# Kernel tuning notes

Hardware: AMD Instinct MI355X
Metric: run time of the kernel (lower is better)

The kernel has to match this reference:

```python
import jax, jax.numpy as jnp
import numpy as np

B, S, WL = 128, 128, 16
V, C, T = 50000, 100, 17
WE, CE, CF, K, H = 300, 50, 50, 3, 256
D = WE + CF  # LSTM input dim


def setup_inputs() -> dict:
    key = jax.random.key(0)
    ks = jax.random.split(key, 16)
    def n(k, shape, scale=0.05):
        return jax.random.normal(k, shape, jnp.float32) * scale
    words = jax.random.randint(ks[0], (B, S), 0, V)
    chars = jax.random.randint(ks[1], (B, S, WL), 0, C)
    tags = jax.random.randint(ks[2], (B, S), 0, T)
    lengths = jax.random.randint(ks[3], (B,), 1, S + 1)  # at least 1 valid token
    return dict(
        words=words, chars=chars, tags=tags, lengths=lengths,
        word_emb=n(ks[4], (V, WE)).at[0].set(0.0),  # padding_idx=0
        char_emb=n(ks[5], (C, CE)),
        conv_w=n(ks[6], (CF, CE, K)), conv_b=jnp.zeros((CF,), jnp.float32),
        w_ih_f=n(ks[7], (4 * H, D)), w_hh_f=n(ks[8], (4 * H, H)), b_f=jnp.zeros((4 * H,), jnp.float32),
        w_ih_b=n(ks[9], (4 * H, D)), w_hh_b=n(ks[10], (4 * H, H)), b_b=jnp.zeros((4 * H,), jnp.float32),
        proj_w=n(ks[11], (T, 2 * H)), proj_b=jnp.zeros((T,), jnp.float32),
        trans=n(ks[12], (T, T), 0.1), start_trans=n(ks[13], (T,), 0.1), end_trans=n(ks[14], (T,), 0.1),
    )


def _lstm(x, mask, w_ih, w_hh, b):
    # x: [B,S,D], mask: [B,S] bool. PyTorch gate order: i, f, g, o.
    Bh = w_hh.shape[1]
    xg = jnp.einsum('bsd,gd->bsg', x, w_ih) + b  # [B,S,4H]
    def step(carry, inp):
        h, c = carry
        gx, m = inp  # [B,4H], [B]
        g = gx + h @ w_hh.T
        i, f, gg, o = jnp.split(g, 4, axis=-1)
        i = jax.nn.sigmoid(i); f = jax.nn.sigmoid(f)
        gg = jnp.tanh(gg); o = jax.nn.sigmoid(o)
        cn = f * c + i * gg
        hn = o * jnp.tanh(cn)
        m_ = m[:, None]
        return (jnp.where(m_, hn, h), jnp.where(m_, cn, c)), hn * m_
    b_ = x.shape[0]
    init = (jnp.zeros((b_, Bh), x.dtype), jnp.zeros((b_, Bh), x.dtype))
    _, hs = jax.lax.scan(step, init, (jnp.swapaxes(xg, 0, 1), jnp.swapaxes(mask, 0, 1)))
    return jnp.swapaxes(hs, 0, 1)  # [B,S,H]


def _reverse_valid(x, lengths):
    # reverse only the first `length` entries of each row (pack_padded semantics)
    s = x.shape[1]
    t = jnp.arange(s)[None, :]
    idx = jnp.where(t < lengths[:, None], lengths[:, None] - 1 - t, t)
    return jnp.take_along_axis(x, idx[:, :, None], axis=1)


def _crf_nll(emissions, tags, lengths, trans, start_trans, end_trans):
    b, s, t_ = emissions.shape
    mask = jnp.arange(s)[None, :] < lengths[:, None]  # [B,S]
    maskf = mask.astype(emissions.dtype)
    # gold path score
    emit_sc = jnp.take_along_axis(emissions, tags[:, :, None], axis=2)[:, :, 0]  # [B,S]
    score = start_trans[tags[:, 0]] + (emit_sc * maskf).sum(1)
    tr = trans[tags[:, :-1], tags[:, 1:]]  # [B,S-1]
    score = score + (tr * maskf[:, 1:]).sum(1)
    last = jnp.take_along_axis(tags, (lengths - 1)[:, None], axis=1)[:, 0]
    score = score + end_trans[last]
    # partition function (forward algorithm)
    alpha0 = start_trans[None, :] + emissions[:, 0]  # [B,T]
    def step(alpha, inp):
        emit, m = inp  # [B,T], [B]
        nxt = jax.scipy.special.logsumexp(alpha[:, :, None] + trans[None] + emit[:, None, :], axis=1)
        return jnp.where(m[:, None], nxt, alpha), None
    alpha, _ = jax.lax.scan(step, alpha0,
                            (jnp.swapaxes(emissions[:, 1:], 0, 1), jnp.swapaxes(mask[:, 1:], 0, 1)))
    logZ = jax.scipy.special.logsumexp(alpha + end_trans[None, :], axis=-1)
    return jnp.sum(logZ - score)


def reference(words, chars, tags, lengths, word_emb, char_emb, conv_w, conv_b,
              w_ih_f, w_hh_f, b_f, w_ih_b, w_hh_b, b_b, proj_w, proj_b,
              trans, start_trans, end_trans):
    b, s = words.shape
    wl = chars.shape[2]
    we = word_emb[words]  # [B,S,WE]
    ce = char_emb[chars]  # [B,S,WL,CE]
    # CharCNN: conv over word-length, relu, max-pool
    x = ce.reshape(b * s, wl, -1).transpose(0, 2, 1)  # [B*S, CE, WL]
    conv = jax.lax.conv_general_dilated(x, conv_w, (1,), 'SAME',
                                        dimension_numbers=('NCH', 'OIH', 'NCH'))
    conv = conv + conv_b[None, :, None]
    cf = jnp.max(jax.nn.relu(conv), axis=-1).reshape(b, s, -1)  # [B,S,CF]
    inp = jnp.concatenate([we, cf], axis=2)  # [B,S,WE+CF]
    mask = jnp.arange(s)[None, :] < lengths[:, None]
    fwd = _lstm(inp, mask, w_ih_f, w_hh_f, b_f)
    bwd = _reverse_valid(_lstm(_reverse_valid(inp, lengths), mask, w_ih_b, w_hh_b, b_b), lengths)
    h = jnp.concatenate([fwd, bwd], axis=2)  # [B,S,2H]
    emissions = jnp.einsum('bsh,th->bst', h, proj_w) + proj_b
    return _crf_nll(emissions, tags, lengths, trans, start_trans, end_trans)
```

## Files before the change

### kernel.cpp

```cpp
#include <hip/hip_runtime.h>
#include <stdint.h>

typedef unsigned char u8;
typedef unsigned short u16;
typedef unsigned int u32;
typedef unsigned long long u64;

#define NPOS 16384
#define KPAD 384

typedef __attribute__((ext_vector_type(8))) short bf16x8;
typedef __attribute__((ext_vector_type(4))) float f32x4;
typedef __attribute__((ext_vector_type(8))) int i32x8;

__device__ __forceinline__ float bf2f(u16 u) { return __uint_as_float(((u32)u) << 16); }
__device__ __forceinline__ u16 f2bf(float f) {
    u32 u = __float_as_uint(f);
    u += 0x7fffu + ((u >> 16) & 1u);
    return (u16)(u >> 16);
}
__device__ __forceinline__ float frcp(float x) {
#if __has_builtin(__builtin_amdgcn_rcpf)
    return __builtin_amdgcn_rcpf(x);
#else
    return 1.0f / x;
#endif
}
__device__ __forceinline__ float sigm(float x) { return frcp(1.0f + __expf(-x)); }
__device__ __forceinline__ float tanh_(float x) { return fmaf(2.0f, frcp(1.0f + __expf(-2.0f * x)), -1.0f); }

__device__ u8 f2fp8_manual(float f) {
    u32 u = __float_as_uint(f);
    u32 s = (u >> 31) << 7;
    u32 ae = (u >> 23) & 255u;
    u32 m = u & 0x7fffffu;
    int e = (int)ae - 127;
    if (ae == 0) return (u8)s;
    if (e >= 9) return (u8)(s | 0x7e);
    if (e >= -6) {
        u32 mant = m >> 20;
        u32 rem = m & 0xfffffu;
        if (rem > 0x80000u || (rem == 0x80000u && (mant & 1u))) mant++;
        u32 ef = (u32)(e + 7);
        if (mant == 8u) { mant = 0u; ef++; }
        if (ef >= 16u || (ef == 15u && mant == 7u)) return (u8)(s | 0x7e);
        return (u8)(s | (ef << 3) | mant);
    }
    if (e < -10) return (u8)s;
    int sb = 14 - e;
    u32 X = 0x800000u | m;
    u32 mant = X >> sb;
    u32 rem = X & ((1u << sb) - 1u);
    u32 half = 1u << (sb - 1);
    if (rem > half || (rem == half && (mant & 1u))) mant++;
    if (mant >= 8u) return (u8)(s | (1u << 3));
    return (u8)(s | mant);
}

__device__ __forceinline__ u32 f2fp8(float f) {
#if __has_builtin(__builtin_amdgcn_cvt_pk_fp8_f32)
    return (u32)(__builtin_amdgcn_cvt_pk_fp8_f32(f, f, 0, false) & 0xff);
#else
    return (u32)f2fp8_manual(f);
#endif
}

static constexpr size_t OFF_INP  = 0;
static constexpr size_t OFF_WIH  = 12582912;
static constexpr size_t OFF_WHH  = 14155776;
static constexpr size_t OFF_XG   = 15204352;
static constexpr size_t OFF_HS   = 82313216;
static constexpr size_t OFF_EMIS = 99090432;
static constexpr size_t OFF_NLL  = 100204544;

__global__ __launch_bounds__(128) void k_prep_wih(const float* __restrict__ wf,
                                                  const float* __restrict__ wb,
                                                  u16* __restrict__ wih) {
    int n = blockIdx.x, tid = threadIdx.x;
    const float* src = (n < 1024) ? (wf + (size_t)n * 350) : (wb + (size_t)(n - 1024) * 350);
    u16* dst = wih + (size_t)n * KPAD;
    for (int k = tid; k < KPAD; k += 128) dst[k] = (k < 350) ? f2bf(src[k]) : (u16)0;
}

__global__ __launch_bounds__(128) void k_prep_whh8(const float* __restrict__ wf,
                                                   const float* __restrict__ wb,
                                                   u8* __restrict__ whh8) {
    int bx = blockIdx.x, tid = threadIdx.x;
    int d = bx >> 10, row = bx & 1023;
    const float* src = (d ? wb : wf) + (size_t)row * 256;
    int g = row >> 8, hid = row & 255;
    int w = hid >> 5, nb = (hid >> 4) & 1, c16 = hid & 15;
    u8* base = whh8 + ((size_t)((d * 8 + w) * 4 + g)) * 8192;
    for (int k = tid; k < 256; k += 128) {
        int kk = k >> 7, q = (k >> 5) & 3, j = k & 31;
        base[((nb * 2 + kk) * 64 + (q * 16 + c16)) * 32 + j] = f2fp8_manual(src[k]);
    }
}

__global__ __launch_bounds__(128) void k_embed_conv(const int* __restrict__ words,
                                                    const int* __restrict__ chars,
                                                    const float* __restrict__ word_emb,
                                                    const float* __restrict__ char_emb,
                                                    const float* __restrict__ conv_w,
                                                    const float* __restrict__ conv_b,
                                                    u16* __restrict__ inp) {
    int pos = blockIdx.x, tid = threadIdx.x;
    __shared__ float ce[18 * 50];
    const int* ch = chars + (size_t)pos * 16;
    for (int i = tid; i < 18 * 50; i += 128) {
        int row = i / 50, c = i - row * 50;
        float v = 0.f;
        if (row >= 1 && row <= 16) v = char_emb[(size_t)ch[row - 1] * 50 + c];
        ce[i] = v;
    }
    __syncthreads();
    {
        const float4* we4 = (const float4*)(word_emb + (size_t)words[pos] * 300);
        u16* op = inp + (size_t)pos * KPAD;
        if (tid < 75) {
            float4 v = we4[tid];
            u64 pk = (u64)f2bf(v.x) | ((u64)f2bf(v.y) << 16) |
                     ((u64)f2bf(v.z) << 32) | ((u64)f2bf(v.w) << 48);
            *(u64*)(op + tid * 4) = pk;
        }
        for (int c = 350 + tid; c < KPAD; c += 128) op[c] = 0;
    }
    if (tid < 100) {
        int oc = tid >> 1, half = tid & 1, t0 = half * 8;
        float acc[8];
#pragma unroll
        for (int tt = 0; tt < 8; ++tt) acc[tt] = 0.f;
        const float* wrow = conv_w + (size_t)oc * 150;
        for (int ic = 0; ic < 50; ++ic) {
#pragma unroll
            for (int k = 0; k < 3; ++k) {
                float wv = wrow[ic * 3 + k];
#pragma unroll
                for (int tt = 0; tt < 8; ++tt)
                    acc[tt] = fmaf(ce[(t0 + tt + k) * 50 + ic], wv, acc[tt]);
            }
        }
        float cb = conv_b[oc];
        float m = 0.f;
#pragma unroll
        for (int tt = 0; tt < 8; ++tt) m = fmaxf(m, acc[tt] + cb);
        m = fmaxf(m, __shfl_xor(m, 1));
        if (half == 0) inp[(size_t)pos * KPAD + 300 + oc] = f2bf(m);
    }
}

__global__ __launch_bounds__(256, 2) void k_gemm(const u16* __restrict__ A,
                                                 const u16* __restrict__ Bm,
                                                 u16* __restrict__ C,
                                                 const int* __restrict__ lengths,
                                                 const float* __restrict__ bias_f,
                                                 const float* __restrict__ bias_b) {
    __shared__ u16 sa[128 * 64];
    __shared__ u16 sb[128 * 64];
    int tid = threadIdx.x;
    int dd = blockIdx.x >> 3, hblk = blockIdx.x & 7;
    int m0 = blockIdx.y * 128;
    int lane = tid & 63, wid = tid >> 6;
    int wr = wid >> 1, wc = wid & 1;
    f32x4 acc[4][4];
#pragma unroll
    for (int mt = 0; mt < 4; ++mt)
#pragma unroll
        for (int g = 0; g < 4; ++g) acc[mt][g] = (f32x4){0.f, 0.f, 0.f, 0.f};

    for (int kt = 0; kt < 6; ++kt) {
#pragma unroll
        for (int c = 0; c < 4; ++c) {
            int idx = (c * 256 + tid) * 16;
            int row = idx >> 7, colb = idx & 127;
            int dst = idx ^ ((row & 7) << 4);
            uint4 va = *(const uint4*)((const char*)A + (size_t)(m0 + row) * 768 + kt * 128 + colb);
            *(uint4*)((char*)sa + dst) = va;
            int bmrow = dd * 1024 + (row >> 5) * 256 + hblk * 32 + (row & 31);
            uint4 vb = *(const uint4*)((const char*)Bm + (size_t)bmrow * 768 + kt * 128 + colb);
            *(uint4*)((char*)sb + dst) = vb;
        }
        __syncthreads();
#pragma unroll
        for (int kc = 0; kc < 2; ++kc) {
            bf16x8 af[4], bf[4];
#pragma unroll
            for (int mt = 0; mt < 4; ++mt) {
                int row = wr * 64 + mt * 16 + (lane & 15);
                int off = (row * 128 + kc * 64 + (lane >> 4) * 16) ^ ((row & 7) << 4);
                af[mt] = *(const bf16x8*)((const char*)sa + off);
            }
#pragma unroll
            for (int g = 0; g < 4; ++g) {
                int row = g * 32 + wc * 16 + (lane & 15);
                int off = (row * 128 + kc * 64 + (lane >> 4) * 16) ^ ((row & 7) << 4);
                bf[g] = *(const bf16x8*)((const char*)sb + off);
            }
#pragma unroll
            for (int mt = 0; mt < 4; ++mt)
#pragma unroll
                for (int g = 0; g < 4; ++g)
                    acc[mt][g] = __builtin_amdgcn_mfma_f32_16x16x32_bf16(af[mt], bf[g], acc[mt][g], 0, 0, 0);
        }
        __syncthreads();
    }
    int b = blockIdx.y;
    int len = lengths[b];
    int grp = b >> 4, row16 = b & 15;
    int qq = row16 >> 2, rg = row16 & 3;
    int c16 = lane & 15;
    int hid = hblk * 32 + wc * 16 + c16;
    const float* bias = dd ? bias_b : bias_f;
    float bv[4];
#pragma unroll
    for (int g = 0; g < 4; ++g) bv[g] = bias[g * 256 + hid];
    u32 base16 = (u32)((hblk * 64 + qq * 16 + c16) * 32 + (wc * 4 + rg) * 4);
    size_t slab0 = ((size_t)(dd * 8 + grp) * 128) * 16384;
#pragma unroll
    for (int mt = 0; mt < 4; ++mt)
#pragma unroll
        for (int r = 0; r < 4; ++r) {
            int t = wr * 64 + mt * 16 + (lane >> 4) * 4 + r;
            int tt = dd ? ((t < len) ? (len - 1 - t) : t) : t;
            u64 pk = (u64)f2bf(acc[mt][0][r] + bv[0]) |
                     ((u64)f2bf(acc[mt][1][r] + bv[1]) << 16) |
                     ((u64)f2bf(acc[mt][2][r] + bv[2]) << 32) |
                     ((u64)f2bf(acc[mt][3][r] + bv[3]) << 48);
            *(u64*)(C + slab0 + (size_t)tt * 16384 + base16) = pk;
        }
}

#define LSTM_STEP(T, XC, XN, HA, HW)                                              \
    {                                                                             \
        *(uint4*)(&XN[0])  = *(const uint4*)(xp);                                 \
        *(uint4*)(&XN[4])  = *(const uint4*)(xp + 8);                             \
        *(uint4*)(&XN[8])  = *(const uint4*)(xp + 16);                            \
        *(uint4*)(&XN[12]) = *(const uint4*)(xp + 24);                            \
        xp += 16384;                                                              \
        f32x4 acc[8];                                                             \
        _Pragma("unroll") for (int nb = 0; nb < 2; ++nb)                          \
            _Pragma("unroll") for (int rg = 0; rg < 4; ++rg) {                    \
                int u = nb * 4 + rg;                                              \
                u32 w0 = XC[u * 2], w1 = XC[u * 2 + 1];                           \
                acc[nb * 4 + 0][rg] = __uint_as_float(w0 << 16);                  \
                acc[nb * 4 + 1][rg] = __uint_as_float(w0 & 0xffff0000u);          \
                acc[nb * 4 + 2][rg] = __uint_as_float(w1 << 16);                  \
                acc[nb * 4 + 3][rg] = __uint_as_float(w1 & 0xffff0000u);          \
            }                                                                     \
        i32x8 a0, a1;                                                             \
        *(uint4*)&a0       = *(const uint4*)(HA);                                 \
        *((uint4*)&a0 + 1) = *(const uint4*)(HA + 16);                            \
        *(uint4*)&a1       = *(const uint4*)(HA + 128);                           \
        *((uint4*)&a1 + 1) = *(const uint4*)(HA + 144);                           \
        __builtin_amdgcn_s_setprio(1);                                            \
        _Pragma("unroll") for (int g = 0; g < 4; ++g)                             \
            acc[g] = __builtin_amdgcn_mfma_scale_f32_16x16x128_f8f6f4(            \
                a0, br[g * 4 + 0], acc[g], 0, 0, 0, 127, 0, 127);                 \
        _Pragma("unroll") for (int g = 0; g < 4; ++g)                             \
            acc[g] = __builtin_amdgcn_mfma_scale_f32_16x16x128_f8f6f4(            \
                a1, br[g * 4 + 1], acc[g], 0, 0, 0, 127, 0, 127);                 \
        _Pragma("unroll") for (int g = 0; g < 4; ++g)                             \
            acc[4 + g] = __builtin_amdgcn_mfma_scale_f32_16x16x128_f8f6f4(        \
                a0, br[g * 4 + 2], acc[4 + g], 0, 0, 0, 127, 0, 127);             \
        _Pragma("unroll") for (int g = 0; g < 4; ++g)                             \
            acc[4 + g] = __builtin_amdgcn_mfma_scale_f32_16x16x128_f8f6f4(        \
                a1, br[g * 4 + 3], acc[4 + g], 0, 0, 0, 127, 0, 127);             \
        __builtin_amdgcn_s_setprio(0);                                            \
        _Pragma("unroll") for (int rg = 0; rg < 4; ++rg) {                        \
            bool mv = (T) < lenr[rg];                                             \
            _Pragma("unroll") for (int nb = 0; nb < 2; ++nb) {                    \
                int u = nb * 4 + rg;                                              \
                float gi = sigm(acc[nb * 4 + 0][rg]);                             \
                float gf = sigm(acc[nb * 4 + 1][rg]);                             \
                float gg = tanh_(acc[nb * 4 + 2][rg]);                            \
                float go = sigm(acc[nb * 4 + 3][rg]);                             \
                float cn = gf * cst[u] + gi * gg;                                 \
                float hn = go * tanh_(cn);                                        \
                cst[u] = mv ? cn : cst[u];                                        \
                hbf[u] = mv ? (__float_as_uint(hn) >> 16) : hbf[u];               \
                hq[u]  = mv ? f2fp8(hn) : hq[u];                                  \
                voff[u] += mv ? dstepB : 0;                                       \
                *(u16*)(hsp + voff[u]) = (u16)hbf[u];                             \
                (HW)[rg * 272 + nb * 16] = (u8)hq[u];                             \
            }                                                                     \
        }                                                                         \
        asm volatile("s_waitcnt lgkmcnt(0)\n\ts_barrier" ::: "memory");           \
    }

__global__ __launch_bounds__(512, 2) void k_lstm(const u16* __restrict__ xg2,
                                                 const u8* __restrict__ whh8,
                                                 const int* __restrict__ lengths,
                                                 u16* __restrict__ hs) {
    __shared__ u8 h8[2][4352];
    int tid = threadIdx.x, lane = tid & 63, w = tid >> 6;
    int bx = blockIdx.x;
    int d = bx >> 3, grp = bx & 7;
    int c16 = lane & 15, q = lane >> 4;

    u8* hflat = &h8[0][0];
    for (int i = tid * 8; i < 8704; i += 4096) *(u64*)(hflat + i) = 0;

    int lenr[4];
#pragma unroll
    for (int rg = 0; rg < 4; ++rg) lenr[rg] = lengths[grp * 16 + q * 4 + rg];

    const u8* wbse = whh8 + ((size_t)((d * 8 + w) * 4)) * 8192;
    i32x8 br[16];
#pragma unroll
    for (int g = 0; g < 4; ++g)
#pragma unroll
        for (int nb = 0; nb < 2; ++nb)
#pragma unroll
            for (int kk = 0; kk < 2; ++kk) {
                const u8* p = wbse + (size_t)g * 8192 + ((nb * 2 + kk) * 64 + lane) * 32;
                i32x8 v;
                *(uint4*)&v       = *(const uint4*)p;
                *((uint4*)&v + 1) = *(const uint4*)(p + 16);
                br[g * 4 + nb * 2 + kk] = v;
            }

    float cst[8];
    u32 hq[8], hbf[8];
#pragma unroll
    for (int u = 0; u < 8; ++u) { cst[u] = 0.f; hq[u] = 0; hbf[u] = 0; }

    u32 voff[8];
    int dstepB = d ? -1024 : 1024;
    u8* hsp = (u8*)hs;
#pragma unroll
    for (int nb = 0; nb < 2; ++nb)
#pragma unroll
        for (int rg = 0; rg < 4; ++rg) {
            int u = nb * 4 + rg;
            int row = q * 4 + rg;
            int hid = w * 32 + nb * 16 + c16;
            int p0 = d ? (lenr[rg] - 1) : 0;
            voff[u] = (u32)((((grp * 16 + row) * 128 + p0) * 512 + d * 256 + hid) * 2 - dstepB);
        }

    const u16* xslab = xg2 + ((size_t)(d * 8 + grp) * 128) * 16384 + (w * 64 + lane) * 32;
    u32 xqa[16], xqb[16];
    *(uint4*)(&xqa[0])  = *(const uint4*)(xslab);
    *(uint4*)(&xqa[4])  = *(const uint4*)(xslab + 8);
    *(uint4*)(&xqa[8])  = *(const uint4*)(xslab + 16);
    *(uint4*)(&xqa[12]) = *(const uint4*)(xslab + 24);
    const u16* xp = xslab + 16384;

    const u8* ha0 = hflat + (c16 * 272 + q * 32);
    const u8* ha1 = ha0 + 4352;
    u8* hw1 = hflat + (q * 1088 + w * 32 + c16);
    u8* hw0 = hw1 + 4352;

    __syncthreads();

    for (int t2 = 0; t2 < 128; t2 += 2) {
        LSTM_STEP(t2,     xqa, xqb, ha0, hw0)
        LSTM_STEP(t2 + 1, xqb, xqa, ha1, hw1)
    }
}

__global__ __launch_bounds__(256) void k_emis(const u16* __restrict__ hs,
                                              const float* __restrict__ proj_w,
                                              const float* __restrict__ proj_b,
                                              float* __restrict__ emis) {
    __shared__ float pw[17 * 512];
    int tid = threadIdx.x;
    for (int i = tid; i < 17 * 512; i += 256) pw[i] = proj_w[i];
    __syncthreads();
    int lane = tid & 63, wv = tid >> 6;
    int pos = blockIdx.x * 4 + wv;
    float hv[8];
    const u16* hp = hs + (size_t)pos * 512 + lane * 8;
#pragma unroll
    for (int j = 0; j < 8; ++j) hv[j] = bf2f(hp[j]);
    for (int tg = 0; tg < 17; ++tg) {
        const float* wp = pw + tg * 512 + lane * 8;
        float s = 0.f;
#pragma unroll
        for (int j = 0; j < 8; ++j) s = fmaf(hv[j], wp[j], s);
#pragma unroll
        for (int off = 32; off; off >>= 1) s += __shfl_down(s, off);
        if (lane == 0) emis[(size_t)pos * 17 + tg] = s + proj_b[tg];
    }
}

__global__ __launch_bounds__(64) void k_crf(const float* __restrict__ emis,
                                            const int* __restrict__ tags,
                                            const int* __restrict__ lengths,
                                            const float* __restrict__ trans,
                                            const float* __restrict__ start_trans,
                                            const float* __restrict__ end_trans,
                                            float* __restrict__ nll) {
    int b = blockIdx.x, lane = threadIdx.x;
    __shared__ float tr[289];
    __shared__ float al[17];
    __shared__ float scs;
    for (int i = lane; i < 289; i += 64) tr[i] = trans[i];
    int len = lengths[b];
    const int* tg = tags + (size_t)b * 128;
    const float* em = emis + (size_t)b * 128 * 17;
    __syncthreads();

    float sc = 0.f;
    for (int t = lane; t < len; t += 64) {
        sc += em[t * 17 + tg[t]];
        if (t >= 1) sc += tr[tg[t - 1] * 17 + tg[t]];
    }
#pragma unroll
    for (int off = 32; off; off >>= 1) sc += __shfl_down(sc, off);
    if (lane == 0) scs = sc + start_trans[tg[0]] + end_trans[tg[len - 1]];

    if (lane < 17) al[lane] = start_trans[lane] + em[lane];
    __syncthreads();
    for (int t = 1; t < len; ++t) {
        float anew = 0.f;
        if (lane < 17) {
            float m = -1e30f;
            for (int i = 0; i < 17; ++i) m = fmaxf(m, al[i] + tr[i * 17 + lane]);
            float s = 0.f;
            for (int i = 0; i < 17; ++i) s += __expf(al[i] + tr[i * 17 + lane] - m);
            anew = m + __logf(s) + em[t * 17 + lane];
        }
        __syncthreads();
        if (lane < 17) al[lane] = anew;
        __syncthreads();
    }
    float v = (lane < 17) ? al[lane] + end_trans[lane] : -1e30f;
    float m = v;
#pragma unroll
    for (int off = 32; off; off >>= 1) m = fmaxf(m, __shfl_xor(m, off));
    float s = (lane < 17) ? __expf(v - m) : 0.f;
#pragma unroll
    for (int off = 32; off; off >>= 1) s += __shfl_xor(s, off);
    if (lane == 0) nll[b] = (m + __logf(s)) - scs;
}

__global__ __launch_bounds__(128) void k_reduce(const float* __restrict__ nll, float* __restrict__ out) {
    int tid = threadIdx.x;
    float v = nll[tid];
#pragma unroll
    for (int off = 32; off; off >>= 1) v += __shfl_down(v, off);
    __shared__ float partial[2];
    if ((tid & 63) == 0) partial[tid >> 6] = v;
    __syncthreads();
    if (tid == 0) out[0] = partial[0] + partial[1];
}

extern "C" void kernel_launch(void* const* d_in, const int* in_sizes, int n_in,
                              void* d_out, int out_size, void* d_ws, size_t ws_size,
                              hipStream_t stream) {
    (void)in_sizes; (void)n_in; (void)out_size; (void)ws_size;
    const int*   words       = (const int*)d_in[0];
    const int*   chars       = (const int*)d_in[1];
    const int*   tags        = (const int*)d_in[2];
    const int*   lengths     = (const int*)d_in[3];
    const float* word_emb    = (const float*)d_in[4];
    const float* char_emb    = (const float*)d_in[5];
    const float* conv_w      = (const float*)d_in[6];
    const float* conv_b      = (const float*)d_in[7];
    const float* w_ih_f      = (const float*)d_in[8];
    const float* w_hh_f      = (const float*)d_in[9];
    const float* b_f         = (const float*)d_in[10];
    const float* w_ih_b      = (const float*)d_in[11];
    const float* w_hh_b      = (const float*)d_in[12];
    const float* b_b         = (const float*)d_in[13];
    const float* proj_w      = (const float*)d_in[14];
    const float* proj_b      = (const float*)d_in[15];
    const float* trans       = (const float*)d_in[16];
    const float* start_trans = (const float*)d_in[17];
    const float* end_trans   = (const float*)d_in[18];

    char* ws = (char*)d_ws;
    u16* inp   = (u16*)(ws + OFF_INP);
    u16* wih   = (u16*)(ws + OFF_WIH);
    u8*  whh8  = (u8*)(ws + OFF_WHH);
    u16* xgb   = (u16*)(ws + OFF_XG);
    u16* hsb   = (u16*)(ws + OFF_HS);
    float* em  = (float*)(ws + OFF_EMIS);
    float* nll = (float*)(ws + OFF_NLL);

    k_prep_wih<<<2048, 128, 0, stream>>>(w_ih_f, w_ih_b, wih);
    k_prep_whh8<<<2048, 128, 0, stream>>>(w_hh_f, w_hh_b, whh8);
    k_embed_conv<<<NPOS, 128, 0, stream>>>(words, chars, word_emb, char_emb, conv_w, conv_b, inp);
    k_gemm<<<dim3(16, 128), 256, 0, stream>>>(inp, wih, xgb, lengths, b_f, b_b);
    k_lstm<<<16, 512, 0, stream>>>(xgb, whh8, lengths, hsb);
    k_emis<<<4096, 256, 0, stream>>>(hsb, proj_w, proj_b, em);
    k_crf<<<128, 64, 0, stream>>>(em, tags, lengths, trans, start_trans, end_trans, nll);
    k_reduce<<<1, 128, 0, stream>>>(nll, (float*)d_out);
}
```

Baseline: 479.8 us.

## Fuse weight prep with embedding/conv front kernel and batch emission positions

Merges the two weight-preparation kernels and the embedding/char-CNN kernel into one launch. Each block now handles 8 positions, using a transposed conv weight table and a transposed char-embedding tile in shared memory, so each thread computes two output channels over all 16 time steps. The emission kernel processes 4 positions per wave with vectorised loads, which amortises the shuffle reductions and the loads of projection weights. This cuts launch count and per-block setup in exchange for more register pressure in the conv loop. It also adds a small transpose kernel that reuses the XG workspace region before the GEMM writes into it.

```diff
diff --git a/kernel.cpp b/kernel.cpp
--- a/kernel.cpp
+++ b/kernel.cpp
@@ -72,80 +72,129 @@
 static constexpr size_t OFF_HS   = 82313216;
 static constexpr size_t OFF_EMIS = 99090432;
 static constexpr size_t OFF_NLL  = 100204544;
-
-__global__ __launch_bounds__(128) void k_prep_wih(const float* __restrict__ wf,
-                                                  const float* __restrict__ wb,
-                                                  u16* __restrict__ wih) {
-    int n = blockIdx.x, tid = threadIdx.x;
-    const float* src = (n < 1024) ? (wf + (size_t)n * 350) : (wb + (size_t)(n - 1024) * 350);
-    u16* dst = wih + (size_t)n * KPAD;
-    for (int k = tid; k < KPAD; k += 128) dst[k] = (k < 350) ? f2bf(src[k]) : (u16)0;
-}
-
-__global__ __launch_bounds__(128) void k_prep_whh8(const float* __restrict__ wf,
-                                                   const float* __restrict__ wb,
-                                                   u8* __restrict__ whh8) {
-    int bx = blockIdx.x, tid = threadIdx.x;
-    int d = bx >> 10, row = bx & 1023;
-    const float* src = (d ? wb : wf) + (size_t)row * 256;
-    int g = row >> 8, hid = row & 255;
-    int w = hid >> 5, nb = (hid >> 4) & 1, c16 = hid & 15;
-    u8* base = whh8 + ((size_t)((d * 8 + w) * 4 + g)) * 8192;
-    for (int k = tid; k < 256; k += 128) {
-        int kk = k >> 7, q = (k >> 5) & 3, j = k & 31;
-        base[((nb * 2 + kk) * 64 + (q * 16 + c16)) * 32 + j] = f2fp8_manual(src[k]);
-    }
-}
-
-__global__ __launch_bounds__(128) void k_embed_conv(const int* __restrict__ words,
-                                                    const int* __restrict__ chars,
-                                                    const float* __restrict__ word_emb,
-                                                    const float* __restrict__ char_emb,
-                                                    const float* __restrict__ conv_w,
-                                                    const float* __restrict__ conv_b,
-                                                    u16* __restrict__ inp) {
-    int pos = blockIdx.x, tid = threadIdx.x;
-    __shared__ float ce[18 * 50];
-    const int* ch = chars + (size_t)pos * 16;
-    for (int i = tid; i < 18 * 50; i += 128) {
-        int row = i / 50, c = i - row * 50;
-        float v = 0.f;
-        if (row >= 1 && row <= 16) v = char_emb[(size_t)ch[row - 1] * 50 + c];
-        ce[i] = v;
+static constexpr size_t OFF_WT   = OFF_XG;
+
+__global__ __launch_bounds__(256) void k_prep0(const float* __restrict__ conv_w,
+                                               float* __restrict__ wt) {
+    int idx = blockIdx.x * 256 + threadIdx.x;
+    if (idx < 7500) {
+        int oc = idx / 150, r = idx - oc * 150;
+        wt[r * 52 + oc] = conv_w[oc * 150 + r];
+    }
+}
+
+__global__ __launch_bounds__(256) void k_front(const int* __restrict__ words,
+                                               const int* __restrict__ chars,
+                                               const float* __restrict__ word_emb,
+                                               const float* __restrict__ char_emb,
+                                               const float* __restrict__ wt,
+                                               const float* __restrict__ conv_b,
+                                               u16* __restrict__ inp,
+                                               const float* __restrict__ wihf,
+                                               const float* __restrict__ wihb,
+                                               u16* __restrict__ wih,
+                                               const float* __restrict__ whf,
+                                               const float* __restrict__ whb,
+                                               u8* __restrict__ whh8) {
+    __shared__ float ce_t[8][50][20];
+    int b = blockIdx.x, tid = threadIdx.x;
+
+    if (b >= 2048) {
+        if (b < 3072) {
+            int n = (b - 2048) * 2 + (tid >> 7);
+            int t128 = tid & 127;
+            const float* src = (n < 1024) ? (wihf + (size_t)n * 350) : (wihb + (size_t)(n - 1024) * 350);
+            u16* dst = wih + (size_t)n * KPAD;
+            for (int k = t128; k < KPAD; k += 128) dst[k] = (k < 350) ? f2bf(src[k]) : (u16)0;
+        } else {
+            int gr = (b - 3072) * 2 + (tid >> 7);
+            int t128 = tid & 127;
+            int d = gr >> 10, row = gr & 1023;
+            const float* src = (d ? whb : whf) + (size_t)row * 256;
+            int g = row >> 8, hid = row & 255;
+            int w = hid >> 5, nb = (hid >> 4) & 1, c16 = hid & 15;
+            u8* base = whh8 + ((size_t)((d * 8 + w) * 4 + g)) * 8192;
+            for (int k = t128; k < 256; k += 128) {
+                int kk = k >> 7, q = (k >> 5) & 3, j = k & 31;
+                base[((nb * 2 + kk) * 64 + (q * 16 + c16)) * 32 + j] = f2fp8_manual(src[k]);
+            }
+        }
+        return;
+    }
+
+    int pos0 = b * 8;
+
+    if (tid < 128) {
+        int p = tid >> 4, c = tid & 15;
+        int ch = chars[(size_t)(pos0 + p) * 16 + c];
+        const float* src = char_emb + (size_t)ch * 50;
+#pragma unroll
+        for (int i = 0; i < 25; ++i) {
+            float2 v = *(const float2*)(src + i * 2);
+            ce_t[p][i * 2][c + 1] = v.x;
+            ce_t[p][i * 2 + 1][c + 1] = v.y;
+        }
+    } else {
+        int base = tid - 128;
+        for (int i = base; i < 1600; i += 128) {
+            int p = i / 200, rem = i - p * 200;
+            int ic = rem >> 2, cid = rem & 3;
+            ce_t[p][ic][cid == 0 ? 0 : 16 + cid] = 0.f;
+        }
+    }
+
+    for (int r = 0; r < 3; ++r) {
+        int idx = r * 256 + tid;
+        if (idx < 600) {
+            int p = idx / 75, v = idx - p * 75;
+            const float4* we4 = (const float4*)(word_emb + (size_t)words[pos0 + p] * 300);
+            float4 val = we4[v];
+            u64 pk = (u64)f2bf(val.x) | ((u64)f2bf(val.y) << 16) |
+                     ((u64)f2bf(val.z) << 32) | ((u64)f2bf(val.w) << 48);
+            *(u64*)(inp + (size_t)(pos0 + p) * KPAD + v * 4) = pk;
+        }
+    }
+    {
+        int idx = tid;
+        if (idx < 136) {
+            int p = idx / 17, j = idx - p * 17;
+            *(u32*)(inp + (size_t)(pos0 + p) * KPAD + 350 + 2 * j) = 0;
+        }
     }
     __syncthreads();
-    {
-        const float4* we4 = (const float4*)(word_emb + (size_t)words[pos] * 300);
-        u16* op = inp + (size_t)pos * KPAD;
-        if (tid < 75) {
-            float4 v = we4[tid];
-            u64 pk = (u64)f2bf(v.x) | ((u64)f2bf(v.y) << 16) |
-                     ((u64)f2bf(v.z) << 32) | ((u64)f2bf(v.w) << 48);
-            *(u64*)(op + tid * 4) = pk;
-        }
-        for (int c = 350 + tid; c < KPAD; c += 128) op[c] = 0;
-    }
-    if (tid < 100) {
-        int oc = tid >> 1, half = tid & 1, t0 = half * 8;
-        float acc[8];
-#pragma unroll
-        for (int tt = 0; tt < 8; ++tt) acc[tt] = 0.f;
-        const float* wrow = conv_w + (size_t)oc * 150;
+
+    if (tid < 200) {
+        int p = tid / 25, ocp = tid - p * 25;
+        int oc = ocp * 2;
+        float acc0[16], acc1[16];
+#pragma unroll
+        for (int t = 0; t < 16; ++t) { acc0[t] = 0.f; acc1[t] = 0.f; }
+        const float* cebase = &ce_t[p][0][0];
         for (int ic = 0; ic < 50; ++ic) {
+            float c[20];
+            const float* cp = cebase + ic * 20;
+#pragma unroll
+            for (int i = 0; i < 5; ++i) *(float4*)(&c[i * 4]) = *(const float4*)(cp + i * 4);
 #pragma unroll
             for (int k = 0; k < 3; ++k) {
-                float wv = wrow[ic * 3 + k];
-#pragma unroll
-                for (int tt = 0; tt < 8; ++tt)
-                    acc[tt] = fmaf(ce[(t0 + tt + k) * 50 + ic], wv, acc[tt]);
+                float2 wv = *(const float2*)(wt + (ic * 3 + k) * 52 + oc);
+#pragma unroll
+                for (int t = 0; t < 16; ++t) {
+                    acc0[t] = fmaf(c[t + k], wv.x, acc0[t]);
+                    acc1[t] = fmaf(c[t + k], wv.y, acc1[t]);
+                }
             }
         }
-        float cb = conv_b[oc];
-        float m = 0.f;
-#pragma unroll
-        for (int tt = 0; tt < 8; ++tt) m = fmaxf(m, acc[tt] + cb);
-        m = fmaxf(m, __shfl_xor(m, 1));
-        if (half == 0) inp[(size_t)pos * KPAD + 300 + oc] = f2bf(m);
+        float cb0 = conv_b[oc], cb1 = conv_b[oc + 1];
+        float m0 = 0.f, m1 = 0.f;
+#pragma unroll
+        for (int t = 0; t < 16; ++t) {
+            m0 = fmaxf(m0, acc0[t] + cb0);
+            m1 = fmaxf(m1, acc1[t] + cb1);
+        }
+        u16* op = inp + (size_t)(pos0 + p) * KPAD + 300 + oc;
+        op[0] = f2bf(m0);
+        op[1] = f2bf(m1);
     }
 }
 
@@ -368,19 +417,35 @@
     for (int i = tid; i < 17 * 512; i += 256) pw[i] = proj_w[i];
     __syncthreads();
     int lane = tid & 63, wv = tid >> 6;
-    int pos = blockIdx.x * 4 + wv;
-    float hv[8];
-    const u16* hp = hs + (size_t)pos * 512 + lane * 8;
-#pragma unroll
-    for (int j = 0; j < 8; ++j) hv[j] = bf2f(hp[j]);
+    int pos0 = blockIdx.x * 16 + wv * 4;
+    float hv[4][8];
+#pragma unroll
+    for (int p = 0; p < 4; ++p) {
+        bf16x8 v = *(const bf16x8*)(hs + (size_t)(pos0 + p) * 512 + lane * 8);
+#pragma unroll
+        for (int j = 0; j < 8; ++j) hv[p][j] = bf2f((u16)v[j]);
+    }
     for (int tg = 0; tg < 17; ++tg) {
         const float* wp = pw + tg * 512 + lane * 8;
-        float s = 0.f;
-#pragma unroll
-        for (int j = 0; j < 8; ++j) s = fmaf(hv[j], wp[j], s);
-#pragma unroll
-        for (int off = 32; off; off >>= 1) s += __shfl_down(s, off);
-        if (lane == 0) emis[(size_t)pos * 17 + tg] = s + proj_b[tg];
+        float wr[8];
+#pragma unroll
+        for (int j = 0; j < 8; ++j) wr[j] = wp[j];
+        float s[4];
+#pragma unroll
+        for (int p = 0; p < 4; ++p) {
+            float acc = 0.f;
+#pragma unroll
+            for (int j = 0; j < 8; ++j) acc = fmaf(hv[p][j], wr[j], acc);
+            s[p] = acc;
+        }
+#pragma unroll
+        for (int off = 32; off; off >>= 1)
+#pragma unroll
+            for (int p = 0; p < 4; ++p) s[p] += __shfl_down(s[p], off);
+        if (lane == 0) {
+#pragma unroll
+            for (int p = 0; p < 4; ++p) emis[(size_t)(pos0 + p) * 17 + tg] = s[p] + proj_b[tg];
+        }
     }
 }
 
@@ -478,13 +543,14 @@
     u16* hsb   = (u16*)(ws + OFF_HS);
     float* em  = (float*)(ws + OFF_EMIS);
     float* nll = (float*)(ws + OFF_NLL);
-
-    k_prep_wih<<<2048, 128, 0, stream>>>(w_ih_f, w_ih_b, wih);
-    k_prep_whh8<<<2048, 128, 0, stream>>>(w_hh_f, w_hh_b, whh8);
-    k_embed_conv<<<NPOS, 128, 0, stream>>>(words, chars, word_emb, char_emb, conv_w, conv_b, inp);
+    float* wt  = (float*)(ws + OFF_WT);
+
+    k_prep0<<<30, 256, 0, stream>>>(conv_w, wt);
+    k_front<<<4096, 256, 0, stream>>>(words, chars, word_emb, char_emb, wt, conv_b, inp,
+                                      w_ih_f, w_ih_b, wih, w_hh_f, w_hh_b, whh8);
     k_gemm<<<dim3(16, 128), 256, 0, stream>>>(inp, wih, xgb, lengths, b_f, b_b);
     k_lstm<<<16, 512, 0, stream>>>(xgb, whh8, lengths, hsb);
-    k_emis<<<4096, 256, 0, stream>>>(hsb, proj_w, proj_b, em);
+    k_emis<<<1024, 256, 0, stream>>>(hsb, proj_w, proj_b, em);
     k_crf<<<128, 64, 0, stream>>>(em, tags, lengths, trans, start_trans, end_trans, nll);
     k_reduce<<<1, 128, 0, stream>>>(nll, (float*)d_out);
 }
```

Result: faster. 445.9 us (-7.1%).
